# Kernel optimization log

Hardware: AMD Instinct MI355X
Metric: run time of the kernel (lower is better)

The kernel has to match this reference:

```python
import jax, jax.numpy as jnp
import numpy as np

B, N, C = 8, 4096, 512

def setup_inputs() -> dict:
    key = jax.random.key(0)
    ks = jax.random.split(key, 6)
    s = 1.0 / np.sqrt(C)
    return {
        "x": jax.random.normal(ks[0], (B, N, C), jnp.float32),
        "Wq": jax.random.normal(ks[1], (C, C), jnp.float32) * s,
        "Wk": jax.random.normal(ks[2], (C, C), jnp.float32) * s,
        "Wv": jax.random.normal(ks[3], (C, C), jnp.float32) * s,
        "W1": jax.random.normal(ks[4], (C, C), jnp.float32) * s,
        "W2": jax.random.normal(ks[5], (C, C), jnp.float32) * s,
    }

def reference(x, Wq, Wk, Wv, W1, W2):
    # torch nn.Linear: y = x @ W.T (bias=False)
    q = x @ Wq.T                      # [B,N,C]
    k = x @ Wk.T
    v = x @ Wv.T
    dim = q.shape[-1]
    q = jax.nn.softmax(q, axis=-1) * (dim ** -0.5)   # softmax over channels
    k = jax.nn.softmax(k, axis=-2)                   # softmax over sequence
    context = jnp.einsum('bnd,bne->bde', k, v)       # [B,C,C]
    attn = jnp.einsum('bnd,bde->bne', q, context)    # [B,N,C]
    x = attn + x
    return (x @ W1.T) @ W2.T + x
```

## Files before the change

### kernel.cpp

```cpp
#include <hip/hip_runtime.h>

typedef unsigned int uint;
typedef __bf16 bf16_t;
typedef bf16_t bf16x8 __attribute__((ext_vector_type(8)));
typedef float floatx4 __attribute__((ext_vector_type(4)));

struct __align__(8) us4 { unsigned short x, y, z, w; };

__device__ __forceinline__ unsigned short f2b(float f) {
    unsigned u = __float_as_uint(f);
    u = u + 0x7FFFu + ((u >> 16) & 1u);
    return (unsigned short)(u >> 16);
}
__device__ __forceinline__ float b2f(unsigned short h) {
    return __uint_as_float(((unsigned)h) << 16);
}

__device__ __forceinline__ void g2l16(const void* g, void* l) {
    __builtin_amdgcn_global_load_lds((__attribute__((address_space(1))) void*)g,
                                     (__attribute__((address_space(3))) void*)l,
                                     16, 0, 0);
}

template <int MODE, int NTN, bool BMS, int LD>
__global__ __launch_bounds__(512, 2) void gemm256(
    const unsigned short* __restrict__ A, const unsigned short* __restrict__ B,
    void* __restrict__ O, const unsigned short* __restrict__ R,
    unsigned short* __restrict__ O2, unsigned short* __restrict__ O3,
    float* __restrict__ Sq, float* __restrict__ Sk,
    const float* __restrict__ Sn,
    int K, long long sB, float scale)
{
    __shared__ __attribute__((aligned(16))) unsigned short Ls[2][4][8192];

    const uint id = blockIdx.x;
    const int tid = threadIdx.x;
    const int l = tid & 63;
    const int w = tid >> 6;
    const int wr = w >> 2;
    const int wc = w & 3;

    int arow0 = 0, n0 = 0, bb = 0;
    const unsigned short* Ab;
    const unsigned short* Bbp;
    long long pbase = 0;

    if constexpr (MODE == 6) {
        const int mt = (int)(id >> 1) & 1, ntc = (int)id & 1;
        const int zz = (int)(id >> 2);
        const int b6 = zz & 7, sk6 = zz >> 3;
        Ab  = A + ((long long)b6 * 512 + mt  * 256) * 4096 + sk6 * 512;
        Bbp = B + ((long long)b6 * 512 + ntc * 256) * 4096 + sk6 * 512;
        pbase = (long long)(b6 * 32 + sk6 * 4 + mt * 2 + ntc) * 65536;
    } else {
        const uint xcd = id & 7;
        const uint g = id >> 3;
        const uint nt = g % NTN;
        const uint mg = g / NTN;
        const uint ms = mg * 8 + xcd;
        if constexpr (BMS) { bb = (int)(ms & 7); arow0 = bb * 4096 + (int)(ms >> 3) * 256; }
        else               { bb = 0;             arow0 = (int)ms * 256; }
        n0 = (int)nt * 256;
        Ab  = A + (long long)arow0 * LD;
        Bbp = B + (long long)bb * sB + (long long)n0 * LD;
    }

    const int n0i = w * 128 + l;
    const int n1i = n0i + 64;
    const unsigned short* pA0 = Ab  + (long long)(n0i >> 2) * LD + ((n0i & 3) ^ ((n0i >> 3) & 3)) * 8;
    const unsigned short* pA1 = Ab  + (long long)(n1i >> 2) * LD + ((n1i & 3) ^ ((n1i >> 3) & 3)) * 8;
    const unsigned short* pB0 = Bbp + (long long)(n0i >> 2) * LD + ((n0i & 3) ^ ((n0i >> 3) & 3)) * 8;
    const unsigned short* pB1 = Bbp + (long long)(n1i >> 2) * LD + ((n1i & 3) ^ ((n1i >> 3) & 3)) * 8;

#define STG(bufi, sl, p0, p1, koff) do {                                    \
        unsigned short* d_ = &Ls[bufi][sl][0] + n0i * 8;                    \
        g2l16((p0) + (koff), d_);                                           \
        g2l16((p1) + (koff), d_ + 512);                                     \
    } while (0)

    const int fr = l & 15;
    const int c0 = l >> 4;
    const int swz = (c0 ^ ((fr >> 1) & 3)) << 4;
    const int aoff = (wr * 128 + fr) * 64 + swz;
    const int boff = (wc * 64 + fr) * 64 + swz;

    floatx4 acc[8][4] = {};
    const int NTk = K >> 6;

    STG(0, 0, pA0, pA1, 0);
    STG(0, 2, pB0, pB1, 0);
    STG(0, 1, pA0, pA1, 32);
    STG(0, 3, pB0, pB1, 32);
    if (NTk > 1) {
        STG(1, 0, pA0, pA1, 64);
        STG(1, 2, pB0, pB1, 64);
    }
    asm volatile("s_waitcnt vmcnt(8)" ::: "memory");
    __builtin_amdgcn_s_barrier();

    for (int t = 0; t < NTk; ++t) {
        const int bi = t & 1;
        const char* Lb = (const char*)&Ls[bi][0][0];
        bf16x8 af[8], bv0, bv1, bv2, bv3;

#pragma unroll
        for (int i = 0; i < 8; ++i)
            af[i] = *(const bf16x8*)(Lb + 0 * 16384 + aoff + i * 1024);
        bv0 = *(const bf16x8*)(Lb + 2 * 16384 + boff);
        bv1 = *(const bf16x8*)(Lb + 2 * 16384 + boff + 1024);
        if (t + 1 < NTk) STG((t + 1) & 1, 1, pA0, pA1, (t + 1) * 64 + 32);
        __builtin_amdgcn_s_barrier();
        __builtin_amdgcn_s_setprio(1);
#pragma unroll
        for (int i = 0; i < 8; ++i) {
            acc[i][0] = __builtin_amdgcn_mfma_f32_16x16x32_bf16(af[i], bv0, acc[i][0], 0, 0, 0);
            acc[i][1] = __builtin_amdgcn_mfma_f32_16x16x32_bf16(af[i], bv1, acc[i][1], 0, 0, 0);
        }
        __builtin_amdgcn_s_setprio(0);
        __builtin_amdgcn_s_barrier();

        bv2 = *(const bf16x8*)(Lb + 2 * 16384 + boff + 2048);
        bv3 = *(const bf16x8*)(Lb + 2 * 16384 + boff + 3072);
        if (t + 1 < NTk) STG((t + 1) & 1, 3, pB0, pB1, (t + 1) * 64 + 32);
        if (t < NTk - 1) asm volatile("s_waitcnt vmcnt(8)" ::: "memory");
        else             asm volatile("s_waitcnt vmcnt(0)" ::: "memory");
        __builtin_amdgcn_s_barrier();
        __builtin_amdgcn_s_setprio(1);
#pragma unroll
        for (int i = 0; i < 8; ++i) {
            acc[i][2] = __builtin_amdgcn_mfma_f32_16x16x32_bf16(af[i], bv2, acc[i][2], 0, 0, 0);
            acc[i][3] = __builtin_amdgcn_mfma_f32_16x16x32_bf16(af[i], bv3, acc[i][3], 0, 0, 0);
        }
        __builtin_amdgcn_s_setprio(0);
        __builtin_amdgcn_s_barrier();

#pragma unroll
        for (int i = 0; i < 8; ++i)
            af[i] = *(const bf16x8*)(Lb + 1 * 16384 + aoff + i * 1024);
        bv0 = *(const bf16x8*)(Lb + 3 * 16384 + boff);
        bv1 = *(const bf16x8*)(Lb + 3 * 16384 + boff + 1024);
        if (t + 2 < NTk) STG(bi, 0, pA0, pA1, (t + 2) * 64);
        __builtin_amdgcn_s_barrier();
        __builtin_amdgcn_s_setprio(1);
#pragma unroll
        for (int i = 0; i < 8; ++i) {
            acc[i][0] = __builtin_amdgcn_mfma_f32_16x16x32_bf16(af[i], bv0, acc[i][0], 0, 0, 0);
            acc[i][1] = __builtin_amdgcn_mfma_f32_16x16x32_bf16(af[i], bv1, acc[i][1], 0, 0, 0);
        }
        __builtin_amdgcn_s_setprio(0);
        __builtin_amdgcn_s_barrier();

        bv2 = *(const bf16x8*)(Lb + 3 * 16384 + boff + 2048);
        bv3 = *(const bf16x8*)(Lb + 3 * 16384 + boff + 3072);
        if (t + 2 < NTk) STG(bi, 2, pB0, pB1, (t + 2) * 64);
        if (t < NTk - 2)       asm volatile("s_waitcnt vmcnt(8)" ::: "memory");
        else if (t == NTk - 2) asm volatile("s_waitcnt vmcnt(4)" ::: "memory");
        __builtin_amdgcn_s_barrier();
        __builtin_amdgcn_s_setprio(1);
#pragma unroll
        for (int i = 0; i < 8; ++i) {
            acc[i][2] = __builtin_amdgcn_mfma_f32_16x16x32_bf16(af[i], bv2, acc[i][2], 0, 0, 0);
            acc[i][3] = __builtin_amdgcn_mfma_f32_16x16x32_bf16(af[i], bv3, acc[i][3], 0, 0, 0);
        }
        __builtin_amdgcn_s_setprio(0);
        __builtin_amdgcn_s_barrier();
    }
#undef STG

    const int col = l & 15;
    const int rbase = (l >> 4) * 4;
    const int gm0 = arow0 + wr * 128 + rbase;
    const int gn0 = n0 + wc * 64 + col;

    if constexpr (MODE == 6) {
        float* Pb = (float*)O + pbase;
#pragma unroll
        for (int i = 0; i < 8; ++i) {
            int lr = wr * 128 + i * 16 + rbase;
#pragma unroll
            for (int j = 0; j < 4; ++j) {
                int lc = wc * 64 + j * 16 + col;
#pragma unroll
                for (int r = 0; r < 4; ++r)
                    Pb[(lr + r) * 256 + lc] = acc[i][j][r];
            }
        }
    } else if constexpr (MODE == 4) {
        if (n0 < 512) {
            unsigned short* Oq = (unsigned short*)O;
            float rs[8][4];
#pragma unroll
            for (int i = 0; i < 8; ++i)
#pragma unroll
                for (int r = 0; r < 4; ++r) rs[i][r] = 0.f;
#pragma unroll
            for (int i = 0; i < 8; ++i) {
                int gm = gm0 + i * 16;
#pragma unroll
                for (int j = 0; j < 4; ++j) {
                    int gn = gn0 + j * 16;
#pragma unroll
                    for (int r = 0; r < 4; ++r) {
                        float e = __expf(acc[i][j][r]);
                        rs[i][r] += e;
                        Oq[(long long)(gm + r) * 512 + gn] = f2b(e);
                    }
                }
            }
#pragma unroll
            for (int i = 0; i < 8; ++i)
#pragma unroll
                for (int r = 0; r < 4; ++r) {
                    float v = rs[i][r];
                    v += __shfl_xor(v, 1);
                    v += __shfl_xor(v, 2);
                    v += __shfl_xor(v, 4);
                    v += __shfl_xor(v, 8);
                    if ((l & 15) == 0)
                        atomicAdd(&Sq[gm0 + i * 16 + r], v);
                }
        } else if (n0 < 1024) {
            const int b = arow0 >> 12;
            const int mq0 = (arow0 & 4095) + wr * 128 + rbase;
            float cs[4] = {0.f, 0.f, 0.f, 0.f};
#pragma unroll
            for (int i = 0; i < 8; ++i) {
                int mq = mq0 + i * 16;
#pragma unroll
                for (int j = 0; j < 4; ++j) {
                    int d = gn0 + j * 16 - 512;
                    float e0 = __expf(acc[i][j][0]);
                    float e1 = __expf(acc[i][j][1]);
                    float e2 = __expf(acc[i][j][2]);
                    float e3 = __expf(acc[i][j][3]);
                    cs[j] += e0 + e1 + e2 + e3;
                    us4 pk = { f2b(e0), f2b(e1), f2b(e2), f2b(e3) };
                    *(us4*)(O2 + ((long long)b * 512 + d) * 4096 + mq) = pk;
                }
            }
#pragma unroll
            for (int j = 0; j < 4; ++j) {
                float v = cs[j];
                v += __shfl_xor(v, 16);
                v += __shfl_xor(v, 32);
                if (l < 16)
                    atomicAdd(&Sk[b * 512 + gn0 + j * 16 - 512], v);
            }
        } else {
            const int b = arow0 >> 12;
            const int mq0 = (arow0 & 4095) + wr * 128 + rbase;
#pragma unroll
            for (int i = 0; i < 8; ++i) {
                int mq = mq0 + i * 16;
#pragma unroll
                for (int j = 0; j < 4; ++j) {
                    int e_ = gn0 + j * 16 - 1024;
                    us4 pk = { f2b(acc[i][j][0]), f2b(acc[i][j][1]),
                               f2b(acc[i][j][2]), f2b(acc[i][j][3]) };
                    *(us4*)(O3 + ((long long)b * 512 + e_) * 4096 + mq) = pk;
                }
            }
        }
    } else if constexpr (MODE == 5) {
#pragma unroll
        for (int i = 0; i < 8; ++i) {
            int gm = gm0 + i * 16;
            float invs[4];
#pragma unroll
            for (int r = 0; r < 4; ++r) invs[r] = scale / Sn[gm + r];
#pragma unroll
            for (int j = 0; j < 4; ++j) {
                int gn = gn0 + j * 16;
#pragma unroll
                for (int r = 0; r < 4; ++r) {
                    long long idx = (long long)(gm + r) * 512 + gn;
                    ((unsigned short*)O)[idx] =
                        f2b(acc[i][j][r] * invs[r] + b2f(R[idx]));
                }
            }
        }
    } else {
#pragma unroll
        for (int i = 0; i < 8; ++i) {
            int gm = gm0 + i * 16;
#pragma unroll
            for (int j = 0; j < 4; ++j) {
                int gn = gn0 + j * 16;
#pragma unroll
                for (int r = 0; r < 4; ++r) {
                    long long idx = (long long)(gm + r) * 512 + gn;
                    float v = acc[i][j][r];
                    if constexpr (MODE == 0) {
                        ((unsigned short*)O)[idx] = f2b(v);
                    } else {
                        ((float*)O)[idx] = v + b2f(R[idx]);
                    }
                }
            }
        }
    }
}

__global__ __launch_bounds__(256) void ctx_reduce(const float* __restrict__ P,
                                                  const float* __restrict__ Sk,
                                                  unsigned short* __restrict__ Ct)
{
    long long f = (long long)blockIdx.x * 256 + threadIdx.x;
    int b = (int)(f >> 16);
    int e = (int)(f >> 7) & 511;
    int d = ((int)f & 127) * 4;
    int mt = e >> 8, nt2 = d >> 8, lr = e & 255, lc = d & 255;
    long long base0 = (long long)(b * 32 + mt * 2 + nt2) * 65536 + lr * 256 + lc;
    float4 s = {0.f, 0.f, 0.f, 0.f};
#pragma unroll
    for (int sp = 0; sp < 8; ++sp) {
        float4 v = *(const float4*)(P + base0 + (long long)sp * 4 * 65536);
        s.x += v.x; s.y += v.y; s.z += v.z; s.w += v.w;
    }
    float4 sk = *(const float4*)(Sk + b * 512 + d);
    us4 o = { f2b(s.x / sk.x), f2b(s.y / sk.y), f2b(s.z / sk.z), f2b(s.w / sk.w) };
    *(us4*)(Ct + ((long long)b * 512 + e) * 512 + d) = o;
}

__global__ __launch_bounds__(256) void f32_to_bf16_k(const float* __restrict__ in,
                                                     unsigned short* __restrict__ out)
{
    long long i = ((long long)blockIdx.x * 256 + threadIdx.x) * 4;
    float4 v = *(const float4*)(in + i);
    us4 o = { f2b(v.x), f2b(v.y), f2b(v.z), f2b(v.w) };
    *(us4*)(out + i) = o;
}

struct WPtrs { const float* in[5]; unsigned short* out[5]; };
__global__ __launch_bounds__(256) void conv_weights(WPtrs p)
{
    int which = blockIdx.y;
    long long i = ((long long)blockIdx.x * 256 + threadIdx.x) * 4;
    float4 v = *(const float4*)(p.in[which] + i);
    us4 o = { f2b(v.x), f2b(v.y), f2b(v.z), f2b(v.w) };
    *(us4*)(p.out[which] + i) = o;
}

__global__ __launch_bounds__(256) void zero_f32(float* __restrict__ p)
{
    long long i = ((long long)blockIdx.x * 256 + threadIdx.x) * 4;
    *(float4*)(p + i) = make_float4(0.f, 0.f, 0.f, 0.f);
}

extern "C" void kernel_launch(void* const* d_in, const int* in_sizes, int n_in,
                              void* d_out, int out_size, void* d_ws, size_t ws_size,
                              hipStream_t stream)
{
    (void)in_sizes; (void)n_in; (void)out_size; (void)ws_size;
    const float* x  = (const float*)d_in[0];
    const float* Wq = (const float*)d_in[1];
    const float* Wk = (const float*)d_in[2];
    const float* Wv = (const float*)d_in[3];
    const float* W1 = (const float*)d_in[4];
    const float* W2 = (const float*)d_in[5];
    float* out = (float*)d_out;

    const int Bn = 8, N = 4096, C = 512;
    const long long M  = (long long)Bn * N;
    const long long XE = M * C;

    char* ws = (char*)d_ws;
    size_t off = 0;
    auto carve = [&](size_t bytes) -> void* {
        void* p = ws + off;
        off += (bytes + 255) & ~(size_t)255;
        return p;
    };

    unsigned short* xb   = (unsigned short*)carve(XE * 2);
    unsigned short* wcat = (unsigned short*)carve((size_t)3 * C * C * 2);
    unsigned short* w1b  = (unsigned short*)carve((size_t)C * C * 2);
    unsigned short* w2b  = (unsigned short*)carve((size_t)C * C * 2);
    unsigned short* q    = (unsigned short*)carve(XE * 2);
    unsigned short* kT   = (unsigned short*)carve(XE * 2);
    unsigned short* vT   = (unsigned short*)carve(XE * 2);
    unsigned short* ctxT = (unsigned short*)carve((size_t)Bn * C * C * 2);
    float* Ssum = (float*)carve((size_t)(M + Bn * C) * 4);
    float* Sq = Ssum;
    float* Sk = Ssum + M;
    unsigned short* xr = kT;
    unsigned short* h  = vT;
    float* P = (float*)d_out;

    zero_f32<<<dim3(36), 256, 0, stream>>>(Ssum);

    f32_to_bf16_k<<<dim3((unsigned)(XE / 1024)), dim3(256), 0, stream>>>(x, xb);
    WPtrs wp = { { Wq, Wk, Wv, W1, W2 },
                 { wcat, wcat + C * C, wcat + 2 * C * C, w1b, w2b } };
    conv_weights<<<dim3((C * C) / 1024, 5), dim3(256), 0, stream>>>(wp);

    gemm256<4, 6, false, 512><<<dim3(768), 512, 0, stream>>>(
        xb, wcat, q, nullptr, kT, vT, Sq, Sk, nullptr, 512, 0, 0.f);

    gemm256<6, 1, false, 4096><<<dim3(256), 512, 0, stream>>>(
        vT, kT, P, nullptr, nullptr, nullptr, nullptr, nullptr, nullptr,
        512, 0, 0.f);
    ctx_reduce<<<dim3(2048), 256, 0, stream>>>(P, Sk, ctxT);

    gemm256<5, 2, true, 512><<<dim3(256), 512, 0, stream>>>(
        q, ctxT, xr, xb, nullptr, nullptr, nullptr, nullptr, Sq,
        512, (long long)C * C, 0.044194173824159216f);

    gemm256<0, 2, false, 512><<<dim3(256), 512, 0, stream>>>(
        xr, w1b, h, nullptr, nullptr, nullptr, nullptr, nullptr, nullptr,
        512, 0, 0.f);

    gemm256<3, 2, false, 512><<<dim3(256), 512, 0, stream>>>(
        h, w2b, out, xr, nullptr, nullptr, nullptr, nullptr, nullptr,
        512, 0, 0.f);
}
```

Baseline: 320.1 us.

## Shrink GEMM tiles to 128x256 with triple-buffered single-barrier pipeline

Replaces the 256x256-tile GEMM with a 128x256 tile, 8 waves each owning 64x64, and a 3-stage LDS ring using one barrier per 32-wide k step instead of four barriers per 64-wide step. Grids double, which gives more blocks per CU and better wave coverage on the 256-CU part, and launch bounds now request 4 blocks per CU. The context partial layout and ctx_reduce indexing are rewritten to match the new tile mapping and XCD-aware slice assignment. The cost is lower arithmetic intensity per tile, so more global and LDS traffic for the B operand, and K is now hardcoded to 512.

```diff
diff --git a/kernel.cpp b/kernel.cpp
--- a/kernel.cpp
+++ b/kernel.cpp
@@ -23,22 +23,22 @@
 }
 
 template <int MODE, int NTN, bool BMS, int LD>
-__global__ __launch_bounds__(512, 2) void gemm256(
+__global__ __launch_bounds__(512, 4) void gemm128(
     const unsigned short* __restrict__ A, const unsigned short* __restrict__ B,
     void* __restrict__ O, const unsigned short* __restrict__ R,
     unsigned short* __restrict__ O2, unsigned short* __restrict__ O3,
     float* __restrict__ Sq, float* __restrict__ Sk,
     const float* __restrict__ Sn,
-    int K, long long sB, float scale)
-{
-    __shared__ __attribute__((aligned(16))) unsigned short Ls[2][4][8192];
+    long long sB, float scale)
+{
+    __shared__ __attribute__((aligned(16))) unsigned short Ls[3][12288];
 
     const uint id = blockIdx.x;
     const int tid = threadIdx.x;
     const int l = tid & 63;
     const int w = tid >> 6;
-    const int wr = w >> 2;
-    const int wc = w & 3;
+    const int wm = (w >> 2) * 64;
+    const int wnb = (w & 3) * 64;
 
     int arow0 = 0, n0 = 0, bb = 0;
     const unsigned short* Ab;
@@ -46,155 +46,112 @@
     long long pbase = 0;
 
     if constexpr (MODE == 6) {
-        const int mt = (int)(id >> 1) & 1, ntc = (int)id & 1;
-        const int zz = (int)(id >> 2);
-        const int b6 = zz & 7, sk6 = zz >> 3;
-        Ab  = A + ((long long)b6 * 512 + mt  * 256) * 4096 + sk6 * 512;
+        const uint xcd = id & 7;
+        const uint g = id >> 3;
+        const int t8 = (int)(g & 7);
+        const int mt = t8 >> 1, ntc = t8 & 1;
+        const int slice = (int)(g >> 3) * 8 + (int)xcd;
+        const int b6 = slice >> 3, sk6 = slice & 7;
+        Ab  = A + ((long long)b6 * 512 + mt  * 128) * 4096 + sk6 * 512;
         Bbp = B + ((long long)b6 * 512 + ntc * 256) * 4096 + sk6 * 512;
-        pbase = (long long)(b6 * 32 + sk6 * 4 + mt * 2 + ntc) * 65536;
+        pbase = (long long)slice * 262144 + (long long)mt * 128 * 512 + ntc * 256;
     } else {
         const uint xcd = id & 7;
         const uint g = id >> 3;
         const uint nt = g % NTN;
         const uint mg = g / NTN;
         const uint ms = mg * 8 + xcd;
-        if constexpr (BMS) { bb = (int)(ms & 7); arow0 = bb * 4096 + (int)(ms >> 3) * 256; }
-        else               { bb = 0;             arow0 = (int)ms * 256; }
+        if constexpr (BMS) { bb = (int)(ms & 7); arow0 = bb * 4096 + (int)(ms >> 3) * 128; }
+        else               { bb = 0;             arow0 = (int)ms * 128; }
         n0 = (int)nt * 256;
         Ab  = A + (long long)arow0 * LD;
         Bbp = B + (long long)bb * sB + (long long)n0 * LD;
     }
 
-    const int n0i = w * 128 + l;
-    const int n1i = n0i + 64;
-    const unsigned short* pA0 = Ab  + (long long)(n0i >> 2) * LD + ((n0i & 3) ^ ((n0i >> 3) & 3)) * 8;
-    const unsigned short* pA1 = Ab  + (long long)(n1i >> 2) * LD + ((n1i & 3) ^ ((n1i >> 3) & 3)) * 8;
-    const unsigned short* pB0 = Bbp + (long long)(n0i >> 2) * LD + ((n0i & 3) ^ ((n0i >> 3) & 3)) * 8;
-    const unsigned short* pB1 = Bbp + (long long)(n1i >> 2) * LD + ((n1i & 3) ^ ((n1i >> 3) & 3)) * 8;
-
-#define STG(bufi, sl, p0, p1, koff) do {                                    \
-        unsigned short* d_ = &Ls[bufi][sl][0] + n0i * 8;                    \
-        g2l16((p0) + (koff), d_);                                           \
-        g2l16((p1) + (koff), d_ + 512);                                     \
+    const int q_ = tid >> 2;
+    const int lc = (tid & 3) ^ ((tid >> 3) & 3);
+    const unsigned short* pA  = Ab  + (long long)q_ * LD + lc * 8;
+    const unsigned short* pB1 = Bbp + (long long)q_ * LD + lc * 8;
+    const unsigned short* pB2 = Bbp + (long long)(128 + q_) * LD + lc * 8;
+
+#define STG(bi, koff) do {                                                  \
+        unsigned short* d_ = &Ls[bi][0] + tid * 8;                          \
+        g2l16(pA  + (koff), d_);                                            \
+        g2l16(pB1 + (koff), d_ + 4096);                                     \
+        g2l16(pB2 + (koff), d_ + 8192);                                     \
     } while (0)
 
     const int fr = l & 15;
     const int c0 = l >> 4;
     const int swz = (c0 ^ ((fr >> 1) & 3)) << 4;
-    const int aoff = (wr * 128 + fr) * 64 + swz;
-    const int boff = (wc * 64 + fr) * 64 + swz;
-
-    floatx4 acc[8][4] = {};
-    const int NTk = K >> 6;
-
-    STG(0, 0, pA0, pA1, 0);
-    STG(0, 2, pB0, pB1, 0);
-    STG(0, 1, pA0, pA1, 32);
-    STG(0, 3, pB0, pB1, 32);
-    if (NTk > 1) {
-        STG(1, 0, pA0, pA1, 64);
-        STG(1, 2, pB0, pB1, 64);
-    }
-    asm volatile("s_waitcnt vmcnt(8)" ::: "memory");
+    const int aoff = (wm + fr) * 64 + swz;
+    const int boff = (128 + wnb + fr) * 64 + swz;
+
+    floatx4 acc[4][4] = {};
+
+    STG(0, 0);
+    STG(1, 32);
+    asm volatile("s_waitcnt vmcnt(3)" ::: "memory");
     __builtin_amdgcn_s_barrier();
 
-    for (int t = 0; t < NTk; ++t) {
-        const int bi = t & 1;
-        const char* Lb = (const char*)&Ls[bi][0][0];
-        bf16x8 af[8], bv0, bv1, bv2, bv3;
-
-#pragma unroll
-        for (int i = 0; i < 8; ++i)
-            af[i] = *(const bf16x8*)(Lb + 0 * 16384 + aoff + i * 1024);
-        bv0 = *(const bf16x8*)(Lb + 2 * 16384 + boff);
-        bv1 = *(const bf16x8*)(Lb + 2 * 16384 + boff + 1024);
-        if (t + 1 < NTk) STG((t + 1) & 1, 1, pA0, pA1, (t + 1) * 64 + 32);
-        __builtin_amdgcn_s_barrier();
+    int cur = 0, stb = 2;
+    for (int t = 0; t < 16; ++t) {
+        if (t + 2 < 16) STG(stb, (t + 2) * 32);
+
+        const char* Lb = (const char*)&Ls[cur][0];
+        bf16x8 af[4], bv[4];
+#pragma unroll
+        for (int i = 0; i < 4; ++i) af[i] = *(const bf16x8*)(Lb + aoff + i * 1024);
+#pragma unroll
+        for (int j = 0; j < 4; ++j) bv[j] = *(const bf16x8*)(Lb + boff + j * 1024);
+
         __builtin_amdgcn_s_setprio(1);
 #pragma unroll
-        for (int i = 0; i < 8; ++i) {
-            acc[i][0] = __builtin_amdgcn_mfma_f32_16x16x32_bf16(af[i], bv0, acc[i][0], 0, 0, 0);
-            acc[i][1] = __builtin_amdgcn_mfma_f32_16x16x32_bf16(af[i], bv1, acc[i][1], 0, 0, 0);
-        }
+        for (int i = 0; i < 4; ++i)
+#pragma unroll
+            for (int j = 0; j < 4; ++j)
+                acc[i][j] = __builtin_amdgcn_mfma_f32_16x16x32_bf16(
+                    af[i], bv[j], acc[i][j], 0, 0, 0);
         __builtin_amdgcn_s_setprio(0);
-        __builtin_amdgcn_s_barrier();
-
-        bv2 = *(const bf16x8*)(Lb + 2 * 16384 + boff + 2048);
-        bv3 = *(const bf16x8*)(Lb + 2 * 16384 + boff + 3072);
-        if (t + 1 < NTk) STG((t + 1) & 1, 3, pB0, pB1, (t + 1) * 64 + 32);
-        if (t < NTk - 1) asm volatile("s_waitcnt vmcnt(8)" ::: "memory");
-        else             asm volatile("s_waitcnt vmcnt(0)" ::: "memory");
-        __builtin_amdgcn_s_barrier();
-        __builtin_amdgcn_s_setprio(1);
-#pragma unroll
-        for (int i = 0; i < 8; ++i) {
-            acc[i][2] = __builtin_amdgcn_mfma_f32_16x16x32_bf16(af[i], bv2, acc[i][2], 0, 0, 0);
-            acc[i][3] = __builtin_amdgcn_mfma_f32_16x16x32_bf16(af[i], bv3, acc[i][3], 0, 0, 0);
-        }
-        __builtin_amdgcn_s_setprio(0);
-        __builtin_amdgcn_s_barrier();
-
-#pragma unroll
-        for (int i = 0; i < 8; ++i)
-            af[i] = *(const bf16x8*)(Lb + 1 * 16384 + aoff + i * 1024);
-        bv0 = *(const bf16x8*)(Lb + 3 * 16384 + boff);
-        bv1 = *(const bf16x8*)(Lb + 3 * 16384 + boff + 1024);
-        if (t + 2 < NTk) STG(bi, 0, pA0, pA1, (t + 2) * 64);
-        __builtin_amdgcn_s_barrier();
-        __builtin_amdgcn_s_setprio(1);
-#pragma unroll
-        for (int i = 0; i < 8; ++i) {
-            acc[i][0] = __builtin_amdgcn_mfma_f32_16x16x32_bf16(af[i], bv0, acc[i][0], 0, 0, 0);
-            acc[i][1] = __builtin_amdgcn_mfma_f32_16x16x32_bf16(af[i], bv1, acc[i][1], 0, 0, 0);
-        }
-        __builtin_amdgcn_s_setprio(0);
-        __builtin_amdgcn_s_barrier();
-
-        bv2 = *(const bf16x8*)(Lb + 3 * 16384 + boff + 2048);
-        bv3 = *(const bf16x8*)(Lb + 3 * 16384 + boff + 3072);
-        if (t + 2 < NTk) STG(bi, 2, pB0, pB1, (t + 2) * 64);
-        if (t < NTk - 2)       asm volatile("s_waitcnt vmcnt(8)" ::: "memory");
-        else if (t == NTk - 2) asm volatile("s_waitcnt vmcnt(4)" ::: "memory");
-        __builtin_amdgcn_s_barrier();
-        __builtin_amdgcn_s_setprio(1);
-#pragma unroll
-        for (int i = 0; i < 8; ++i) {
-            acc[i][2] = __builtin_amdgcn_mfma_f32_16x16x32_bf16(af[i], bv2, acc[i][2], 0, 0, 0);
-            acc[i][3] = __builtin_amdgcn_mfma_f32_16x16x32_bf16(af[i], bv3, acc[i][3], 0, 0, 0);
-        }
-        __builtin_amdgcn_s_setprio(0);
-        __builtin_amdgcn_s_barrier();
+
+        if (t < 15) {
+            if (t < 14) asm volatile("s_waitcnt vmcnt(3)" ::: "memory");
+            else        asm volatile("s_waitcnt vmcnt(0)" ::: "memory");
+            __builtin_amdgcn_s_barrier();
+        }
+        cur = (cur == 2) ? 0 : cur + 1;
+        stb = (stb == 2) ? 0 : stb + 1;
     }
 #undef STG
 
     const int col = l & 15;
     const int rbase = (l >> 4) * 4;
-    const int gm0 = arow0 + wr * 128 + rbase;
-    const int gn0 = n0 + wc * 64 + col;
+    const int gm0 = arow0 + wm + rbase;
+    const int gn0 = n0 + wnb + col;
 
     if constexpr (MODE == 6) {
         float* Pb = (float*)O + pbase;
 #pragma unroll
-        for (int i = 0; i < 8; ++i) {
-            int lr = wr * 128 + i * 16 + rbase;
+        for (int i = 0; i < 4; ++i) {
+            int lr = wm + i * 16 + rbase;
 #pragma unroll
             for (int j = 0; j < 4; ++j) {
-                int lc = wc * 64 + j * 16 + col;
+                int lcc = wnb + j * 16 + col;
 #pragma unroll
                 for (int r = 0; r < 4; ++r)
-                    Pb[(lr + r) * 256 + lc] = acc[i][j][r];
+                    Pb[(long long)(lr + r) * 512 + lcc] = acc[i][j][r];
             }
         }
     } else if constexpr (MODE == 4) {
         if (n0 < 512) {
             unsigned short* Oq = (unsigned short*)O;
-            float rs[8][4];
-#pragma unroll
-            for (int i = 0; i < 8; ++i)
+            float rs[4][4];
+#pragma unroll
+            for (int i = 0; i < 4; ++i)
 #pragma unroll
                 for (int r = 0; r < 4; ++r) rs[i][r] = 0.f;
 #pragma unroll
-            for (int i = 0; i < 8; ++i) {
+            for (int i = 0; i < 4; ++i) {
                 int gm = gm0 + i * 16;
 #pragma unroll
                 for (int j = 0; j < 4; ++j) {
@@ -208,7 +165,7 @@
                 }
             }
 #pragma unroll
-            for (int i = 0; i < 8; ++i)
+            for (int i = 0; i < 4; ++i)
 #pragma unroll
                 for (int r = 0; r < 4; ++r) {
                     float v = rs[i][r];
@@ -221,10 +178,10 @@
                 }
         } else if (n0 < 1024) {
             const int b = arow0 >> 12;
-            const int mq0 = (arow0 & 4095) + wr * 128 + rbase;
+            const int mq0 = (arow0 & 4095) + wm + rbase;
             float cs[4] = {0.f, 0.f, 0.f, 0.f};
 #pragma unroll
-            for (int i = 0; i < 8; ++i) {
+            for (int i = 0; i < 4; ++i) {
                 int mq = mq0 + i * 16;
 #pragma unroll
                 for (int j = 0; j < 4; ++j) {
@@ -248,9 +205,9 @@
             }
         } else {
             const int b = arow0 >> 12;
-            const int mq0 = (arow0 & 4095) + wr * 128 + rbase;
-#pragma unroll
-            for (int i = 0; i < 8; ++i) {
+            const int mq0 = (arow0 & 4095) + wm + rbase;
+#pragma unroll
+            for (int i = 0; i < 4; ++i) {
                 int mq = mq0 + i * 16;
 #pragma unroll
                 for (int j = 0; j < 4; ++j) {
@@ -263,7 +220,7 @@
         }
     } else if constexpr (MODE == 5) {
 #pragma unroll
-        for (int i = 0; i < 8; ++i) {
+        for (int i = 0; i < 4; ++i) {
             int gm = gm0 + i * 16;
             float invs[4];
 #pragma unroll
@@ -281,7 +238,7 @@
         }
     } else {
 #pragma unroll
-        for (int i = 0; i < 8; ++i) {
+        for (int i = 0; i < 4; ++i) {
             int gm = gm0 + i * 16;
 #pragma unroll
             for (int j = 0; j < 4; ++j) {
@@ -306,20 +263,19 @@
                                                   unsigned short* __restrict__ Ct)
 {
     long long f = (long long)blockIdx.x * 256 + threadIdx.x;
-    int b = (int)(f >> 16);
-    int e = (int)(f >> 7) & 511;
-    int d = ((int)f & 127) * 4;
-    int mt = e >> 8, nt2 = d >> 8, lr = e & 255, lc = d & 255;
-    long long base0 = (long long)(b * 32 + mt * 2 + nt2) * 65536 + lr * 256 + lc;
+    long long base = f * 4;
+    int b = (int)(base >> 18);
+    int rem = (int)(base & 262143);
+    int d = rem & 511;
     float4 s = {0.f, 0.f, 0.f, 0.f};
 #pragma unroll
     for (int sp = 0; sp < 8; ++sp) {
-        float4 v = *(const float4*)(P + base0 + (long long)sp * 4 * 65536);
+        float4 v = *(const float4*)(P + (long long)(b * 8 + sp) * 262144 + rem);
         s.x += v.x; s.y += v.y; s.z += v.z; s.w += v.w;
     }
     float4 sk = *(const float4*)(Sk + b * 512 + d);
     us4 o = { f2b(s.x / sk.x), f2b(s.y / sk.y), f2b(s.z / sk.z), f2b(s.w / sk.w) };
-    *(us4*)(Ct + ((long long)b * 512 + e) * 512 + d) = o;
+    *(us4*)(Ct + (long long)b * 262144 + rem) = o;
 }
 
 __global__ __launch_bounds__(256) void f32_to_bf16_k(const float* __restrict__ in,
@@ -394,23 +350,23 @@
                  { wcat, wcat + C * C, wcat + 2 * C * C, w1b, w2b } };
     conv_weights<<<dim3((C * C) / 1024, 5), dim3(256), 0, stream>>>(wp);
 
-    gemm256<4, 6, false, 512><<<dim3(768), 512, 0, stream>>>(
-        xb, wcat, q, nullptr, kT, vT, Sq, Sk, nullptr, 512, 0, 0.f);
-
-    gemm256<6, 1, false, 4096><<<dim3(256), 512, 0, stream>>>(
+    gemm128<4, 6, false, 512><<<dim3(1536), 512, 0, stream>>>(
+        xb, wcat, q, nullptr, kT, vT, Sq, Sk, nullptr, 0, 0.f);
+
+    gemm128<6, 1, false, 4096><<<dim3(512), 512, 0, stream>>>(
         vT, kT, P, nullptr, nullptr, nullptr, nullptr, nullptr, nullptr,
-        512, 0, 0.f);
+        0, 0.f);
     ctx_reduce<<<dim3(2048), 256, 0, stream>>>(P, Sk, ctxT);
 
-    gemm256<5, 2, true, 512><<<dim3(256), 512, 0, stream>>>(
+    gemm128<5, 2, true, 512><<<dim3(512), 512, 0, stream>>>(
         q, ctxT, xr, xb, nullptr, nullptr, nullptr, nullptr, Sq,
-        512, (long long)C * C, 0.044194173824159216f);
-
-    gemm256<0, 2, false, 512><<<dim3(256), 512, 0, stream>>>(
+        (long long)C * C, 0.044194173824159216f);
+
+    gemm128<0, 2, false, 512><<<dim3(512), 512, 0, stream>>>(
         xr, w1b, h, nullptr, nullptr, nullptr, nullptr, nullptr, nullptr,
-        512, 0, 0.f);
-
-    gemm256<3, 2, false, 512><<<dim3(256), 512, 0, stream>>>(
+        0, 0.f);
+
+    gemm128<3, 2, false, 512><<<dim3(512), 512, 0, stream>>>(
         h, w2b, out, xr, nullptr, nullptr, nullptr, nullptr, nullptr,
-        512, 0, 0.f);
-}
+        0, 0.f);
+}
```

New measurement: 303.2 us. 1.06x faster.
